# Performance work log

Measured on AMD Instinct MI355X. Metric: run time of the kernel, lower is better.

The kernel has to match this reference:

```python
import jax, jax.numpy as jnp
import numpy as np

D_MODEL = 1024
N_HEADS = 16
NUM_KV_HEADS = 4
D_K = D_MODEL // N_HEADS
ROPE_BASE = 10000.0


def apply_rotary_emb(x, base):
    # x: (B, H, T, d) ; rotate interleaved pairs (x[2i], x[2i+1])
    B, H, T, d = x.shape
    inv_freq = 1.0 / (base ** (jnp.arange(0, d, 2, dtype=jnp.float32) / d))  # (d/2,)
    angles = jnp.arange(T, dtype=jnp.float32)[:, None] * inv_freq[None, :]   # (T, d/2)
    cos = jnp.cos(angles)[None, None]  # (1,1,T,d/2)
    sin = jnp.sin(angles)[None, None]
    x1 = x[..., 0::2]
    x2 = x[..., 1::2]
    out = jnp.stack([x1 * cos - x2 * sin, x1 * sin + x2 * cos], axis=-1)
    return out.reshape(B, H, T, d)


def setup_inputs() -> dict:
    key = jax.random.key(0)
    k1, k2, k3, k4, k5 = jax.random.split(key, 5)
    B, T = 4, 2048
    s = 1.0 / np.sqrt(D_MODEL)
    return {
        "x": jax.random.normal(k1, (B, T, D_MODEL), dtype=jnp.float32),
        "attention_mask": jnp.ones((B, T), dtype=jnp.int32),
        "Wq": jax.random.uniform(k2, (D_MODEL, D_MODEL), jnp.float32, -s, s),
        "Wk": jax.random.uniform(k3, (D_MODEL, NUM_KV_HEADS * D_K), jnp.float32, -s, s),
        "Wv": jax.random.uniform(k4, (D_MODEL, NUM_KV_HEADS * D_K), jnp.float32, -s, s),
        "Wo": jax.random.uniform(k5, (D_MODEL, D_MODEL), jnp.float32, -s, s),
    }


def reference(x, attention_mask, Wq, Wk, Wv, Wo):
    B, T, _ = x.shape
    # QKV projections -> (B, H, T, d_k)
    Q = (x @ Wq).reshape(B, T, N_HEADS, D_K).transpose(0, 2, 1, 3)
    K = (x @ Wk).reshape(B, T, NUM_KV_HEADS, D_K).transpose(0, 2, 1, 3)
    V = (x @ Wv).reshape(B, T, NUM_KV_HEADS, D_K).transpose(0, 2, 1, 3)
    # RoPE on Q and K
    Q = apply_rotary_emb(Q, ROPE_BASE)
    K = apply_rotary_emb(K, ROPE_BASE)
    # GQA expansion: repeat kv heads to match query heads
    rep = N_HEADS // NUM_KV_HEADS
    K = jnp.repeat(K, rep, axis=1)
    V = jnp.repeat(V, rep, axis=1)
    # mask: causal AND query-position padding (faithful to source's pad[:,None,:,None])
    causal = jnp.tril(jnp.ones((T, T), dtype=bool))[None, None]        # (1,1,T,T)
    pad = attention_mask.astype(bool)[:, None, :, None]                 # (B,1,T,1)
    mask = pad & causal                                                 # (B,1,T,T)
    scale = 1.0 / np.sqrt(D_K)
    scores = jnp.einsum("bhqd,bhkd->bhqk", Q, K) * scale
    scores = jnp.where(mask, scores, jnp.finfo(scores.dtype).min)
    attn = jax.nn.softmax(scores, axis=-1)
    out = jnp.einsum("bhqk,bhkd->bhqd", attn, V)                       # (B,H,T,d_k)
    out = out.transpose(0, 2, 1, 3).reshape(B, T, D_MODEL)
    return out @ Wo
```

## Files before the change

### kernel.cpp

```cpp
#include <hip/hip_runtime.h>
#include <hip/hip_bf16.h>


#define B_   4
#define T_   2048
#define DM   1024
#define NH   16
#define NKV  4
#define DK   64
#define BT   (B_ * T_)
#define DKV  (NKV * DK)

typedef __attribute__((ext_vector_type(4))) short s4;
typedef __attribute__((ext_vector_type(8))) short s8;
typedef __attribute__((ext_vector_type(4))) float f4;
typedef __attribute__((ext_vector_type(16))) float f16x;

#define L2E    1.4426950408889634f
#define L2_1E4 0.41524101186092307f

__device__ __forceinline__ unsigned short f2bf(float f) {
    __hip_bfloat16 h = __float2bfloat16(f);
    unsigned short u; __builtin_memcpy(&u, &h, 2); return u;
}
__device__ __forceinline__ float bf2f(unsigned short u) {
    __hip_bfloat16 h; __builtin_memcpy(&h, &u, 2); return __bfloat162float(h);
}

__device__ __forceinline__ float ldf(const void* p, size_t i, bool f32) {
    return f32 ? ((const float*)p)[i]
               : __bfloat162float(((const __hip_bfloat16*)p)[i]);
}
__device__ __forceinline__ bool world_f32(const int* flag) {
    return __builtin_amdgcn_readfirstlane(flag[0]) == 0;
}

__device__ __forceinline__ void async_cp16(const unsigned short* g, unsigned short* l) {
    __builtin_amdgcn_global_load_lds(
        (const __attribute__((address_space(1))) void*)g,
        (__attribute__((address_space(3))) void*)l,
        16, 0, 0);
}

__global__ void probe_fmt(const unsigned int* __restrict__ x, int* __restrict__ flag)
{
    __shared__ int cnt;
    if (threadIdx.x == 0) cnt = 0;
    __syncthreads();
    int local = 0;
    #pragma unroll
    for (int i = 0; i < 16; ++i) {
        unsigned int w  = x[threadIdx.x * 16 + i];
        unsigned int lo = w & 0xFFFFu;
        unsigned int e  = (lo >> 7) & 0xFFu;
        if ((lo & 0x7FFFu) == 0u || (e >= 96u && e <= 144u)) ++local;
    }
    atomicAdd(&cnt, local);
    __syncthreads();
    if (threadIdx.x == 0) flag[0] = (cnt >= 3072) ? 1 : 0;
}

__global__ __launch_bounds__(256) void cvt_x(const float* __restrict__ x,
                                             unsigned short* __restrict__ xb,
                                             const int* __restrict__ flag)
{
    if (!world_f32(flag)) return;
    const size_t i = ((size_t)blockIdx.x * 256 + threadIdx.x) * 8;
    f4 a = *(const f4*)(x + i);
    f4 b = *(const f4*)(x + i + 4);
    unsigned short h[8] = { f2bf(a.x), f2bf(a.y), f2bf(a.z), f2bf(a.w),
                            f2bf(b.x), f2bf(b.y), f2bf(b.z), f2bf(b.w) };
    __builtin_memcpy(xb + i, h, 16);
}

__global__ __launch_bounds__(256) void transp2(const void* __restrict__ W0,
                                               const void* __restrict__ W1,
                                               unsigned short* __restrict__ T0,
                                               unsigned short* __restrict__ T1,
                                               int K, int N,
                                               const int* __restrict__ flag)
{
    const bool f32 = world_f32(flag);
    __shared__ unsigned short Tl[32][33];
    const void* W = blockIdx.z ? W1 : W0;
    unsigned short* T = blockIdx.z ? T1 : T0;
    const int n0 = blockIdx.x * 32, k0 = blockIdx.y * 32;
    const int tx = threadIdx.x & 31, ty = threadIdx.x >> 5;
    #pragma unroll
    for (int i = 0; i < 4; ++i)
        Tl[ty + 8 * i][tx] = f2bf(ldf(W, (size_t)(k0 + ty + 8 * i) * N + n0 + tx, f32));
    __syncthreads();
    #pragma unroll
    for (int i = 0; i < 4; ++i)
        T[(size_t)(n0 + ty + 8 * i) * K + k0 + tx] = Tl[tx][ty + 8 * i];
}

__global__ __launch_bounds__(256) void gemm_bt(const unsigned short* __restrict__ A0,
                                               const unsigned short* __restrict__ A1,
                                               const unsigned short* __restrict__ Bt,
                                               void* __restrict__ C,
                                               void* __restrict__ C2,
                                               int M, int N, int K,
                                               const int* __restrict__ flag,
                                               int mode, float rope_scale)
{
    const unsigned short* Ab = world_f32(flag) ? A1 : A0;

    __shared__ unsigned short Al[3][128 * 32];
    __shared__ unsigned short Bl[3][128 * 32];

    const int tid  = threadIdx.x;
    const int bm   = blockIdx.y * 128;
    const int bn   = blockIdx.x * 128;
    const int w    = tid >> 6;
    const int lane = tid & 63;
    const int qd   = lane >> 4;
    const int ln   = lane & 15;
    const int wm   = (w & 1) * 64;
    const int wn   = (w >> 1) * 64;
    const int sr   = tid >> 2;
    const int sk   = (tid & 3) * 8;

#define STAGE(bb, k0_) {                                                                 \
    async_cp16(Ab + (size_t)(bm + sr) * K + (k0_) + sk,      &Al[bb][tid * 8]);          \
    async_cp16(Ab + (size_t)(bm + 64 + sr) * K + (k0_) + sk, &Al[bb][2048 + tid * 8]);   \
    async_cp16(Bt + (size_t)(bn + sr) * K + (k0_) + sk,      &Bl[bb][tid * 8]);          \
    async_cp16(Bt + (size_t)(bn + 64 + sr) * K + (k0_) + sk, &Bl[bb][2048 + tid * 8]);   \
}

    f4 zero = {0.f, 0.f, 0.f, 0.f};
    f4 acc[4][4];
    #pragma unroll
    for (int i = 0; i < 4; ++i)
        #pragma unroll
        for (int j = 0; j < 4; ++j) acc[i][j] = zero;

    const int NS = K >> 5;
    STAGE(0, 0)
    STAGE(1, 32)
    for (int s = 0; s < NS; ++s) {
        const int cur = s % 3;
        if (s + 1 < NS) asm volatile("s_waitcnt vmcnt(4)" ::: "memory");
        else            asm volatile("s_waitcnt vmcnt(0)" ::: "memory");
        if (s + 2 < NS) { STAGE((s + 2) % 3, (s + 2) << 5) }
        asm volatile("s_barrier" ::: "memory");

        s8 af[4], bfr[4];
        #pragma unroll
        for (int i = 0; i < 4; ++i)
            af[i] = *(const s8*)&Al[cur][(wm + 16 * i + ln) * 32 + qd * 8];
        #pragma unroll
        for (int j = 0; j < 4; ++j)
            bfr[j] = *(const s8*)&Bl[cur][(wn + 16 * j + ln) * 32 + qd * 8];
        #pragma unroll
        for (int i = 0; i < 4; ++i)
            #pragma unroll
            for (int j = 0; j < 4; ++j)
                acc[i][j] = __builtin_amdgcn_mfma_f32_16x16x32_bf16(af[i], bfr[j], acc[i][j], 0, 0, 0);
        asm volatile("s_barrier" ::: "memory");
    }
#undef STAGE

    if (mode == 3) {
        #pragma unroll
        for (int j = 0; j < 4; ++j) {
            const int col = bn + wn + 16 * j + ln;
            if (col < 1280) {
                const float scale = (col < 1024) ? rope_scale : 1.0f;
                const int pr = (col >> 1) & 31;
                const float invf = exp2f(-(float)pr * L2_1E4);
                const bool odd = col & 1;
                #pragma unroll
                for (int i = 0; i < 4; ++i)
                    #pragma unroll
                    for (int r = 0; r < 4; ++r) {
                        const int row = bm + wm + 16 * i + qd * 4 + r;
                        float v = acc[i][j][r];
                        float pv = __shfl_xor(v, 1);
                        float ang = (float)(row & (T_ - 1)) * invf;
                        float sn, cs;
                        __sincosf(ang, &sn, &cs);
                        float out = odd ? (pv * sn + v * cs) : (v * cs - pv * sn);
                        acc[i][j][r] = out * scale;
                    }
            }
        }
    }

    #pragma unroll
    for (int i = 0; i < 4; ++i)
        #pragma unroll
        for (int r = 0; r < 4; ++r) {
            const int row = bm + wm + 16 * i + qd * 4 + r;
            #pragma unroll
            for (int j = 0; j < 4; ++j) {
                const int col = bn + wn + 16 * j + ln;
                const float v = acc[i][j][r];
                if (mode == 0) {
                    ((unsigned short*)C)[(size_t)row * N + col] = f2bf(v);
                } else {
                    if (col < 1024) {
                        ((unsigned short*)C)[(size_t)row * DM + col] = f2bf(v);
                    } else {
                        unsigned short* kv = (unsigned short*)C2 +
                            (col < 1280 ? 0 : (size_t)BT * DKV);
                        kv[(size_t)row * DKV + (col & 255)] = f2bf(v);
                    }
                }
            }
        }
}

__global__ __launch_bounds__(256, 3) void attn_mfma(unsigned short* __restrict__ QO,
                                                    const unsigned short* __restrict__ Kg,
                                                    const unsigned short* __restrict__ Vg)
{
    __shared__ unsigned short Kl[64][72];
    __shared__ unsigned short Vl[64][72];

    const int ip   = blockIdx.x;
    const int bh   = blockIdx.y;
    const int b    = bh >> 4;
    const int h    = bh & 15;
    const int hkv  = h >> 2;
    const int tid  = threadIdx.x;
    const int w    = tid >> 6;
    const int lane = tid & 63;
    const int q    = lane & 31;
    const int hl   = lane >> 5;

    const int rk = tid >> 2, dk = (tid & 3) * 16;
    const int kp = tid & 31, vd0 = (tid >> 5) * 8;
    const unsigned short* kptr = Kg + (size_t)(b * T_ + rk) * DKV + hkv * DK + dk;
    const unsigned short* vptr = Vg + (size_t)(b * T_ + 2 * kp) * DKV + hkv * DK + vd0;

    #pragma unroll 1
    for (int seg = 0; seg < 2; ++seg) {
        const int qt    = seg ? ip : (15 - ip);
        const int qb    = qt * 128;
        const int ktmax = 2 * qt + 1;

        uint4 kra0 = ((const uint4*)kptr)[0];
        uint4 kra1 = ((const uint4*)kptr)[1];
        uint4 vra0 = *(const uint4*)vptr;
        uint4 vra1 = *(const uint4*)(vptr + DKV);

        s8 qf[4];
        {
            const unsigned short* Qp =
                QO + (size_t)(b * T_ + qb + 32 * w + q) * DM + h * DK + 8 * hl;
            #pragma unroll
            for (int s = 0; s < 4; ++s)
                qf[s] = *(const s8*)(Qp + 16 * s);
        }

        const int qmaxw = qb + 32 * w + 31;
        const int qglob = qb + 32 * w + q;

        f16x O0, O1;
        #pragma unroll
        for (int r = 0; r < 16; ++r) { O0[r] = 0.f; O1[r] = 0.f; }
        float lsumA = 0.f, lsumB = 0.f;

        for (int kt = 0; kt <= ktmax; ++kt) {
            *(uint4*)&Kl[rk][dk]     = kra0;
            *(uint4*)&Kl[rk][dk + 8] = kra1;
            {
                const unsigned short* lo = (const unsigned short*)&vra0;
                const unsigned short* hi = (const unsigned short*)&vra1;
                #pragma unroll
                for (int i = 0; i < 8; ++i)
                    *(unsigned int*)&Vl[vd0 + i][2 * kp] =
                        (unsigned int)lo[i] | ((unsigned int)hi[i] << 16);
            }
            if (kt < ktmax) {
                const size_t o = (size_t)(kt + 1) * 64 * DKV;
                kra0 = ((const uint4*)(kptr + o))[0];
                kra1 = ((const uint4*)(kptr + o))[1];
                vra0 = *(const uint4*)(vptr + o);
                vra1 = *(const uint4*)(vptr + o + DKV);
            }
            asm volatile("s_waitcnt lgkmcnt(0)\n\ts_barrier" ::: "memory");

            const int kb = kt * 64;
            if (kb <= qmaxw) {
                f16x S0, S1;
                #pragma unroll
                for (int r = 0; r < 16; ++r) { S0[r] = 0.f; S1[r] = 0.f; }
                #pragma unroll
                for (int s = 0; s < 4; ++s) {
                    s8 k0 = *(const s8*)&Kl[q][16 * s + 8 * hl];
                    s8 k1 = *(const s8*)&Kl[32 + q][16 * s + 8 * hl];
                    S0 = __builtin_amdgcn_mfma_f32_32x32x16_bf16(k0, qf[s], S0, 0, 0, 0);
                    S1 = __builtin_amdgcn_mfma_f32_32x32x16_bf16(k1, qf[s], S1, 0, 0, 0);
                }

                unsigned pk0[8], pk1[8];
                const bool full = (kb + 63 <= qb + 32 * w);
                if (full) {
                    #pragma unroll
                    for (int j = 0; j < 8; ++j) {
                        float a0 = exp2f(S0[2 * j]), a1 = exp2f(S0[2 * j + 1]);
                        float c0 = exp2f(S1[2 * j]), c1 = exp2f(S1[2 * j + 1]);
                        lsumA += a0 + a1;
                        lsumB += c0 + c1;
                        pk0[j] = (unsigned)f2bf(a0) | ((unsigned)f2bf(a1) << 16);
                        pk1[j] = (unsigned)f2bf(c0) | ((unsigned)f2bf(c1) << 16);
                    }
                } else {
                    #pragma unroll
                    for (int j = 0; j < 8; ++j) {
                        const int r0 = 2 * j;
                        const int key0 = kb + (r0 & 3) + 8 * (r0 >> 2) + 4 * hl;
                        float a0 = (key0      <= qglob) ? exp2f(S0[r0])     : 0.f;
                        float a1 = (key0 + 1  <= qglob) ? exp2f(S0[r0 + 1]) : 0.f;
                        float c0 = (key0 + 32 <= qglob) ? exp2f(S1[r0])     : 0.f;
                        float c1 = (key0 + 33 <= qglob) ? exp2f(S1[r0 + 1]) : 0.f;
                        lsumA += a0 + a1;
                        lsumB += c0 + c1;
                        pk0[j] = (unsigned)f2bf(a0) | ((unsigned)f2bf(a1) << 16);
                        pk1[j] = (unsigned)f2bf(c0) | ((unsigned)f2bf(c1) << 16);
                    }
                }

                #define PV_STEP(PG, KS) {                                          \
                    const unsigned a0 = PG[4 * ((KS) & 1) + 0];                    \
                    const unsigned a1 = PG[4 * ((KS) & 1) + 1];                    \
                    const unsigned a2 = PG[4 * ((KS) & 1) + 2];                    \
                    const unsigned a3 = PG[4 * ((KS) & 1) + 3];                    \
                    const unsigned own0 = hl ? a2 : a0;                            \
                    const unsigned own1 = hl ? a3 : a1;                            \
                    const unsigned xs0  = hl ? a0 : a2;                            \
                    const unsigned xs1  = hl ? a1 : a3;                            \
                    const unsigned xa = (unsigned)__shfl_xor((int)xs0, 32);        \
                    const unsigned xb = (unsigned)__shfl_xor((int)xs1, 32);        \
                    unsigned dw[4];                                                \
                    dw[0] = hl ? xa : own0;                                        \
                    dw[1] = hl ? xb : own1;                                        \
                    dw[2] = hl ? own0 : xa;                                        \
                    dw[3] = hl ? own1 : xb;                                        \
                    s8 pf; __builtin_memcpy(&pf, dw, 16);                          \
                    s8 v0 = *(const s8*)&Vl[q][16 * (KS) + 8 * hl];                \
                    s8 v1 = *(const s8*)&Vl[32 + q][16 * (KS) + 8 * hl];           \
                    O0 = __builtin_amdgcn_mfma_f32_32x32x16_bf16(v0, pf, O0, 0, 0, 0); \
                    O1 = __builtin_amdgcn_mfma_f32_32x32x16_bf16(v1, pf, O1, 0, 0, 0); \
                }
                PV_STEP(pk0, 0)
                PV_STEP(pk0, 1)
                PV_STEP(pk1, 2)
                PV_STEP(pk1, 3)
                #undef PV_STEP
            }
            asm volatile("s_barrier" ::: "memory");
        }

        const float lsum = lsumA + lsumB;
        const float lf = lsum + __shfl_xor(lsum, 32);
        const float inv = 1.0f / lf;
        unsigned short* Op = QO + (size_t)(b * T_ + qb + 32 * w + q) * DM + h * DK;
        #pragma unroll
        for (int g2 = 0; g2 < 2; ++g2) {
            #pragma unroll
            for (int rq = 0; rq < 4; ++rq) {
                const int d0 = 32 * g2 + 8 * rq + 4 * hl;
                const float o0 = (g2 ? O1[4 * rq + 0] : O0[4 * rq + 0]) * inv;
                const float o1 = (g2 ? O1[4 * rq + 1] : O0[4 * rq + 1]) * inv;
                const float o2 = (g2 ? O1[4 * rq + 2] : O0[4 * rq + 2]) * inv;
                const float o3 = (g2 ? O1[4 * rq + 3] : O0[4 * rq + 3]) * inv;
                unsigned out2[2] = {
                    (unsigned)f2bf(o0) | ((unsigned)f2bf(o1) << 16),
                    (unsigned)f2bf(o2) | ((unsigned)f2bf(o3) << 16) };
                __builtin_memcpy(Op + d0, out2, 8);
            }
        }
    }
}

__global__ __launch_bounds__(256) void copy_out(const unsigned short* __restrict__ Cb,
                                                void* __restrict__ out,
                                                const int* __restrict__ flag)
{
    const bool f32 = world_f32(flag);
    size_t i = ((size_t)blockIdx.x * 256 + threadIdx.x) * 8;
    uint4 v = *(const uint4*)(Cb + i);
    if (!f32) {
        *(uint4*)((unsigned short*)out + i) = v;
    } else {
        const unsigned short* u = (const unsigned short*)&v;
        float* o = (float*)out + i;
        #pragma unroll
        for (int k = 0; k < 8; ++k) o[k] = bf2f(u[k]);
    }
}

extern "C" void kernel_launch(void* const* d_in, const int* in_sizes, int n_in,
                              void* d_out, int out_size, void* d_ws, size_t ws_size,
                              hipStream_t stream)
{
    const void* x  = d_in[0];
    const void* Wq = d_in[2];
    const void* Wk = d_in[3];
    const void* Wv = d_in[4];
    const void* Wo = d_in[5];

    int* flag = (int*)d_ws;
    unsigned short* WqkvT = (unsigned short*)((char*)d_ws + 4096);
    unsigned short* WoT   = WqkvT + (size_t)1536 * DM;
    unsigned short* Kb    = WoT + (size_t)DM * DM;
    unsigned short* Vb    = Kb + (size_t)BT * DKV;
    unsigned short* Cb    = Kb;

    unsigned short* Qb = (unsigned short*)d_out;
    unsigned short* xb = (unsigned short*)d_out + (size_t)BT * DM;

    dim3 blk(256);

    probe_fmt<<<1, blk, 0, stream>>>((const unsigned int*)x, flag);

    cvt_x<<<dim3(BT * DM / 2048), blk, 0, stream>>>((const float*)x, xb, flag);

    transp2<<<dim3(32, 32, 2), blk, 0, stream>>>(Wq, Wo, WqkvT, WoT, DM, DM, flag);
    transp2<<<dim3(8, 32, 2), blk, 0, stream>>>(
        Wk, Wv, WqkvT + (size_t)1024 * DM, WqkvT + (size_t)1280 * DM, DM, DKV, flag);

    gemm_bt<<<dim3(1536 / 128, BT / 128), blk, 0, stream>>>(
        (const unsigned short*)x, xb, WqkvT, Qb, Kb, BT, 1536, DM, flag, 3, 0.125f * L2E);

    attn_mfma<<<dim3(T_ / 256, B_ * NH), blk, 0, stream>>>(Qb, Kb, Vb);

    gemm_bt<<<dim3(DM / 128, BT / 128), blk, 0, stream>>>(
        Qb, Qb, WoT, Cb, nullptr, BT, DM, DM, flag, 0, 1.0f);
    copy_out<<<dim3(BT * DM / 2048), blk, 0, stream>>>(Cb, d_out, flag);
}
```

Measured before the change: 264.9 us.

## Retile projection GEMMs to 256x256 blocks with 512 threads and k64 double buffering

Replaces the 128x128, 256-thread GEMM (three-stage pipeline over k=32 steps) with a 256x256, 512-thread kernel. Each wave now computes a 128x64 sub-tile, and the kernel double-buffers k=64 slabs in LDS. The aim is more data reuse per LDS load and fewer barrier and pipeline steps per unit of MFMA work. The cost is about 128KB of LDS per block and far fewer blocks: 192 for the QKV GEMM and 128 for the output GEMM. That likely leaves many CUs idle and limits latency hiding to one block per CU.

```diff
diff --git a/kernel.cpp b/kernel.cpp
--- a/kernel.cpp
+++ b/kernel.cpp
@@ -95,86 +95,91 @@
         T[(size_t)(n0 + ty + 8 * i) * K + k0 + tx] = Tl[tx][ty + 8 * i];
 }
 
-__global__ __launch_bounds__(256) void gemm_bt(const unsigned short* __restrict__ A0,
-                                               const unsigned short* __restrict__ A1,
-                                               const unsigned short* __restrict__ Bt,
-                                               void* __restrict__ C,
-                                               void* __restrict__ C2,
-                                               int M, int N, int K,
-                                               const int* __restrict__ flag,
-                                               int mode, float rope_scale)
+__global__ __launch_bounds__(512, 2) void gemm256(const unsigned short* __restrict__ A0,
+                                                  const unsigned short* __restrict__ A1,
+                                                  const unsigned short* __restrict__ Bt,
+                                                  void* __restrict__ C,
+                                                  void* __restrict__ C2,
+                                                  int M, int N, int K,
+                                                  const int* __restrict__ flag,
+                                                  int mode, float rope_scale)
 {
     const unsigned short* Ab = world_f32(flag) ? A1 : A0;
 
-    __shared__ unsigned short Al[3][128 * 32];
-    __shared__ unsigned short Bl[3][128 * 32];
+    __shared__ unsigned short Al[2][256 * 64];
+    __shared__ unsigned short Bl[2][256 * 64];
 
     const int tid  = threadIdx.x;
-    const int bm   = blockIdx.y * 128;
-    const int bn   = blockIdx.x * 128;
+    const int bm   = blockIdx.y * 256;
+    const int bn   = blockIdx.x * 256;
     const int w    = tid >> 6;
+    const int wm   = w >> 2;
+    const int wn   = w & 3;
     const int lane = tid & 63;
     const int qd   = lane >> 4;
     const int ln   = lane & 15;
-    const int wm   = (w & 1) * 64;
-    const int wn   = (w >> 1) * 64;
     const int sr   = tid >> 2;
     const int sk   = (tid & 3) * 8;
 
-#define STAGE(bb, k0_) {                                                                 \
-    async_cp16(Ab + (size_t)(bm + sr) * K + (k0_) + sk,      &Al[bb][tid * 8]);          \
-    async_cp16(Ab + (size_t)(bm + 64 + sr) * K + (k0_) + sk, &Al[bb][2048 + tid * 8]);   \
-    async_cp16(Bt + (size_t)(bn + sr) * K + (k0_) + sk,      &Bl[bb][tid * 8]);          \
-    async_cp16(Bt + (size_t)(bn + 64 + sr) * K + (k0_) + sk, &Bl[bb][2048 + tid * 8]);   \
+#define STAGE(bb, k0_) {                                                                        \
+    async_cp16(Ab + (size_t)(bm + sr) * K + (k0_) + sk,            &Al[bb][sr * 32 + sk]);              \
+    async_cp16(Ab + (size_t)(bm + 128 + sr) * K + (k0_) + sk,      &Al[bb][4096 + sr * 32 + sk]);       \
+    async_cp16(Ab + (size_t)(bm + sr) * K + (k0_) + 32 + sk,       &Al[bb][8192 + sr * 32 + sk]);       \
+    async_cp16(Ab + (size_t)(bm + 128 + sr) * K + (k0_) + 32 + sk, &Al[bb][12288 + sr * 32 + sk]);      \
+    async_cp16(Bt + (size_t)(bn + sr) * K + (k0_) + sk,            &Bl[bb][sr * 32 + sk]);              \
+    async_cp16(Bt + (size_t)(bn + 128 + sr) * K + (k0_) + sk,      &Bl[bb][4096 + sr * 32 + sk]);       \
+    async_cp16(Bt + (size_t)(bn + sr) * K + (k0_) + 32 + sk,       &Bl[bb][8192 + sr * 32 + sk]);       \
+    async_cp16(Bt + (size_t)(bn + 128 + sr) * K + (k0_) + 32 + sk, &Bl[bb][12288 + sr * 32 + sk]);      \
 }
 
     f4 zero = {0.f, 0.f, 0.f, 0.f};
-    f4 acc[4][4];
+    f4 acc[8][4];
     #pragma unroll
-    for (int i = 0; i < 4; ++i)
+    for (int i = 0; i < 8; ++i)
         #pragma unroll
         for (int j = 0; j < 4; ++j) acc[i][j] = zero;
 
-    const int NS = K >> 5;
+    const int NT = K >> 6;
     STAGE(0, 0)
-    STAGE(1, 32)
-    for (int s = 0; s < NS; ++s) {
-        const int cur = s % 3;
-        if (s + 1 < NS) asm volatile("s_waitcnt vmcnt(4)" ::: "memory");
-        else            asm volatile("s_waitcnt vmcnt(0)" ::: "memory");
-        if (s + 2 < NS) { STAGE((s + 2) % 3, (s + 2) << 5) }
+    for (int t = 0; t < NT; ++t) {
+        const int cur = t & 1;
+        asm volatile("s_waitcnt vmcnt(0)" ::: "memory");
         asm volatile("s_barrier" ::: "memory");
-
-        s8 af[4], bfr[4];
-        #pragma unroll
-        for (int i = 0; i < 4; ++i)
-            af[i] = *(const s8*)&Al[cur][(wm + 16 * i + ln) * 32 + qd * 8];
-        #pragma unroll
-        for (int j = 0; j < 4; ++j)
-            bfr[j] = *(const s8*)&Bl[cur][(wn + 16 * j + ln) * 32 + qd * 8];
-        #pragma unroll
-        for (int i = 0; i < 4; ++i)
+        if (t + 1 < NT) { STAGE(cur ^ 1, (t + 1) << 6) }
+
+        s8 bfr[2][4];
+        #pragma unroll
+        for (int ksub = 0; ksub < 2; ++ksub)
             #pragma unroll
             for (int j = 0; j < 4; ++j)
-                acc[i][j] = __builtin_amdgcn_mfma_f32_16x16x32_bf16(af[i], bfr[j], acc[i][j], 0, 0, 0);
-        asm volatile("s_barrier" ::: "memory");
+                bfr[ksub][j] = *(const s8*)&Bl[cur][ksub * 8192 + (wn * 64 + 16 * j + ln) * 32 + qd * 8];
+        #pragma unroll
+        for (int i = 0; i < 8; ++i) {
+            s8 a0 = *(const s8*)&Al[cur][          (wm * 128 + 16 * i + ln) * 32 + qd * 8];
+            s8 a1 = *(const s8*)&Al[cur][8192 + (wm * 128 + 16 * i + ln) * 32 + qd * 8];
+            #pragma unroll
+            for (int j = 0; j < 4; ++j) {
+                acc[i][j] = __builtin_amdgcn_mfma_f32_16x16x32_bf16(a0, bfr[0][j], acc[i][j], 0, 0, 0);
+                acc[i][j] = __builtin_amdgcn_mfma_f32_16x16x32_bf16(a1, bfr[1][j], acc[i][j], 0, 0, 0);
+            }
+        }
     }
 #undef STAGE
 
     if (mode == 3) {
         #pragma unroll
         for (int j = 0; j < 4; ++j) {
-            const int col = bn + wn + 16 * j + ln;
+            const int col = bn + wn * 64 + 16 * j + ln;
             if (col < 1280) {
                 const float scale = (col < 1024) ? rope_scale : 1.0f;
                 const int pr = (col >> 1) & 31;
                 const float invf = exp2f(-(float)pr * L2_1E4);
                 const bool odd = col & 1;
                 #pragma unroll
-                for (int i = 0; i < 4; ++i)
+                for (int i = 0; i < 8; ++i)
                     #pragma unroll
                     for (int r = 0; r < 4; ++r) {
-                        const int row = bm + wm + 16 * i + qd * 4 + r;
+                        const int row = bm + wm * 128 + 16 * i + qd * 4 + r;
                         float v = acc[i][j][r];
                         float pv = __shfl_xor(v, 1);
                         float ang = (float)(row & (T_ - 1)) * invf;
@@ -188,13 +193,13 @@
     }
 
     #pragma unroll
-    for (int i = 0; i < 4; ++i)
+    for (int i = 0; i < 8; ++i)
         #pragma unroll
         for (int r = 0; r < 4; ++r) {
-            const int row = bm + wm + 16 * i + qd * 4 + r;
+            const int row = bm + wm * 128 + 16 * i + qd * 4 + r;
             #pragma unroll
             for (int j = 0; j < 4; ++j) {
-                const int col = bn + wn + 16 * j + ln;
+                const int col = bn + wn * 64 + 16 * j + ln;
                 const float v = acc[i][j][r];
                 if (mode == 0) {
                     ((unsigned short*)C)[(size_t)row * N + col] = f2bf(v);
@@ -423,12 +428,12 @@
     transp2<<<dim3(8, 32, 2), blk, 0, stream>>>(
         Wk, Wv, WqkvT + (size_t)1024 * DM, WqkvT + (size_t)1280 * DM, DM, DKV, flag);
 
-    gemm_bt<<<dim3(1536 / 128, BT / 128), blk, 0, stream>>>(
+    gemm256<<<dim3(1536 / 256, BT / 256), dim3(512), 0, stream>>>(
         (const unsigned short*)x, xb, WqkvT, Qb, Kb, BT, 1536, DM, flag, 3, 0.125f * L2E);
 
     attn_mfma<<<dim3(T_ / 256, B_ * NH), blk, 0, stream>>>(Qb, Kb, Vb);
 
-    gemm_bt<<<dim3(DM / 128, BT / 128), blk, 0, stream>>>(
+    gemm256<<<dim3(DM / 256, BT / 256), dim3(512), 0, stream>>>(
         Qb, Qb, WoT, Cb, nullptr, BT, DM, DM, flag, 0, 1.0f);
     copy_out<<<dim3(BT * DM / 2048), blk, 0, stream>>>(Cb, d_out, flag);
 }
```

Result: slower. 292.5 us (+10.4%).

## Split long causal query tiles across blocks with partial-sum combine kernel

Applied to the files above, without the earlier changes.

Replaces the paired-segment attention schedule with a 22-slot work table per (batch, head). The largest query tiles (10-15) are split over two blocks that each process half the key range and write unnormalized fp32 partial outputs and row sums, which a new combine kernel adds and normalizes. The occupancy hint rises from 3 to 5 blocks per CU. The aim is better load balance and more parallelism across CUs, at the cost of extra fp32 scratch traffic, an extra launch, and workspace reuse of the weight and x buffers. Splitting only happens on the fp32 input path; otherwise the split slots exit early.

```diff
diff --git a/kernel.cpp b/kernel.cpp
--- a/kernel.cpp
+++ b/kernel.cpp
@@ -211,18 +211,39 @@
         }
 }
 
-__global__ __launch_bounds__(256, 3) void attn_mfma(unsigned short* __restrict__ QO,
+__global__ __launch_bounds__(256, 5) void attn_mfma(unsigned short* __restrict__ QO,
                                                     const unsigned short* __restrict__ Kg,
-                                                    const unsigned short* __restrict__ Vg)
+                                                    const unsigned short* __restrict__ Vg,
+                                                    const int* __restrict__ flag,
+                                                    float* __restrict__ pA,
+                                                    float* __restrict__ pB,
+                                                    float* __restrict__ lA,
+                                                    float* __restrict__ lB)
 {
     __shared__ unsigned short Kl[64][72];
     __shared__ unsigned short Vl[64][72];
 
-    const int ip   = blockIdx.x;
-    const int bh   = blockIdx.y;
+    const int TQT[22]  = {9,8,15,15,7,14,14,13,13,6,12,12,11,11,5,10,10,4,3,2,1,0};
+    const int TLO[22]  = {0,0,0,16,0,0,15,0,14,0,0,13,0,12,0,0,11,0,0,0,0,0};
+    const int THI[22]  = {19,17,15,31,15,14,29,13,27,13,12,25,11,23,11,10,21,9,7,5,3,1};
+    const int TMODE[22]= {0,0,1,2,0,1,2,1,2,0,1,2,1,2,0,1,2,0,0,0,0,0};
+
+    const bool wf32 = world_f32(flag);
+    const int bh   = blockIdx.x;
+    const int slot = blockIdx.y;
+    const int qt   = TQT[slot];
+    const int lo   = TLO[slot];
+    int hi   = THI[slot];
+    int mode = TMODE[slot];
+    if (!wf32) {
+        if (mode == 2) return;
+        if (mode == 1) { hi = 2 * qt + 1; mode = 0; }
+    }
+
     const int b    = bh >> 4;
     const int h    = bh & 15;
     const int hkv  = h >> 2;
+    const int qb   = qt * 128;
     const int tid  = threadIdx.x;
     const int w    = tid >> 6;
     const int lane = tid & 63;
@@ -231,131 +252,126 @@
 
     const int rk = tid >> 2, dk = (tid & 3) * 16;
     const int kp = tid & 31, vd0 = (tid >> 5) * 8;
-    const unsigned short* kptr = Kg + (size_t)(b * T_ + rk) * DKV + hkv * DK + dk;
-    const unsigned short* vptr = Vg + (size_t)(b * T_ + 2 * kp) * DKV + hkv * DK + vd0;
-
-    #pragma unroll 1
-    for (int seg = 0; seg < 2; ++seg) {
-        const int qt    = seg ? ip : (15 - ip);
-        const int qb    = qt * 128;
-        const int ktmax = 2 * qt + 1;
-
-        uint4 kra0 = ((const uint4*)kptr)[0];
-        uint4 kra1 = ((const uint4*)kptr)[1];
-        uint4 vra0 = *(const uint4*)vptr;
-        uint4 vra1 = *(const uint4*)(vptr + DKV);
-
-        s8 qf[4];
+    const unsigned short* kptr = Kg + (size_t)(b * T_ + lo * 64 + rk) * DKV + hkv * DK + dk;
+    const unsigned short* vptr = Vg + (size_t)(b * T_ + lo * 64 + 2 * kp) * DKV + hkv * DK + vd0;
+
+    uint4 kra0 = ((const uint4*)kptr)[0];
+    uint4 kra1 = ((const uint4*)kptr)[1];
+    uint4 vra0 = *(const uint4*)vptr;
+    uint4 vra1 = *(const uint4*)(vptr + DKV);
+
+    s8 qf[4];
+    {
+        const unsigned short* Qp =
+            QO + (size_t)(b * T_ + qb + 32 * w + q) * DM + h * DK + 8 * hl;
+        #pragma unroll
+        for (int s = 0; s < 4; ++s)
+            qf[s] = *(const s8*)(Qp + 16 * s);
+    }
+
+    const int qmaxw = qb + 32 * w + 31;
+    const int qglob = qb + 32 * w + q;
+
+    f16x O0, O1;
+    #pragma unroll
+    for (int r = 0; r < 16; ++r) { O0[r] = 0.f; O1[r] = 0.f; }
+    float lsumA = 0.f, lsumB = 0.f;
+
+    for (int kt = lo; kt <= hi; ++kt) {
+        *(uint4*)&Kl[rk][dk]     = kra0;
+        *(uint4*)&Kl[rk][dk + 8] = kra1;
         {
-            const unsigned short* Qp =
-                QO + (size_t)(b * T_ + qb + 32 * w + q) * DM + h * DK + 8 * hl;
-            #pragma unroll
-            for (int s = 0; s < 4; ++s)
-                qf[s] = *(const s8*)(Qp + 16 * s);
-        }
-
-        const int qmaxw = qb + 32 * w + 31;
-        const int qglob = qb + 32 * w + q;
-
-        f16x O0, O1;
-        #pragma unroll
-        for (int r = 0; r < 16; ++r) { O0[r] = 0.f; O1[r] = 0.f; }
-        float lsumA = 0.f, lsumB = 0.f;
-
-        for (int kt = 0; kt <= ktmax; ++kt) {
-            *(uint4*)&Kl[rk][dk]     = kra0;
-            *(uint4*)&Kl[rk][dk + 8] = kra1;
-            {
-                const unsigned short* lo = (const unsigned short*)&vra0;
-                const unsigned short* hi = (const unsigned short*)&vra1;
+            const unsigned short* lov = (const unsigned short*)&vra0;
+            const unsigned short* hiv = (const unsigned short*)&vra1;
+            #pragma unroll
+            for (int i = 0; i < 8; ++i)
+                *(unsigned int*)&Vl[vd0 + i][2 * kp] =
+                    (unsigned int)lov[i] | ((unsigned int)hiv[i] << 16);
+        }
+        if (kt < hi) {
+            const size_t o = (size_t)(kt + 1 - lo) * 64 * DKV;
+            kra0 = ((const uint4*)(kptr + o))[0];
+            kra1 = ((const uint4*)(kptr + o))[1];
+            vra0 = *(const uint4*)(vptr + o);
+            vra1 = *(const uint4*)(vptr + o + DKV);
+        }
+        asm volatile("s_waitcnt lgkmcnt(0)\n\ts_barrier" ::: "memory");
+
+        const int kb = kt * 64;
+        if (kb <= qmaxw) {
+            f16x S0, S1;
+            #pragma unroll
+            for (int r = 0; r < 16; ++r) { S0[r] = 0.f; S1[r] = 0.f; }
+            #pragma unroll
+            for (int s = 0; s < 4; ++s) {
+                s8 k0 = *(const s8*)&Kl[q][16 * s + 8 * hl];
+                s8 k1 = *(const s8*)&Kl[32 + q][16 * s + 8 * hl];
+                S0 = __builtin_amdgcn_mfma_f32_32x32x16_bf16(k0, qf[s], S0, 0, 0, 0);
+                S1 = __builtin_amdgcn_mfma_f32_32x32x16_bf16(k1, qf[s], S1, 0, 0, 0);
+            }
+
+            unsigned pk0[8], pk1[8];
+            const bool full = (kb + 63 <= qb + 32 * w);
+            if (full) {
                 #pragma unroll
-                for (int i = 0; i < 8; ++i)
-                    *(unsigned int*)&Vl[vd0 + i][2 * kp] =
-                        (unsigned int)lo[i] | ((unsigned int)hi[i] << 16);
-            }
-            if (kt < ktmax) {
-                const size_t o = (size_t)(kt + 1) * 64 * DKV;
-                kra0 = ((const uint4*)(kptr + o))[0];
-                kra1 = ((const uint4*)(kptr + o))[1];
-                vra0 = *(const uint4*)(vptr + o);
-                vra1 = *(const uint4*)(vptr + o + DKV);
-            }
-            asm volatile("s_waitcnt lgkmcnt(0)\n\ts_barrier" ::: "memory");
-
-            const int kb = kt * 64;
-            if (kb <= qmaxw) {
-                f16x S0, S1;
+                for (int j = 0; j < 8; ++j) {
+                    float a0 = exp2f(S0[2 * j]), a1 = exp2f(S0[2 * j + 1]);
+                    float c0 = exp2f(S1[2 * j]), c1 = exp2f(S1[2 * j + 1]);
+                    lsumA += a0 + a1;
+                    lsumB += c0 + c1;
+                    pk0[j] = (unsigned)f2bf(a0) | ((unsigned)f2bf(a1) << 16);
+                    pk1[j] = (unsigned)f2bf(c0) | ((unsigned)f2bf(c1) << 16);
+                }
+            } else {
                 #pragma unroll
-                for (int r = 0; r < 16; ++r) { S0[r] = 0.f; S1[r] = 0.f; }
-                #pragma unroll
-                for (int s = 0; s < 4; ++s) {
-                    s8 k0 = *(const s8*)&Kl[q][16 * s + 8 * hl];
-                    s8 k1 = *(const s8*)&Kl[32 + q][16 * s + 8 * hl];
-                    S0 = __builtin_amdgcn_mfma_f32_32x32x16_bf16(k0, qf[s], S0, 0, 0, 0);
-                    S1 = __builtin_amdgcn_mfma_f32_32x32x16_bf16(k1, qf[s], S1, 0, 0, 0);
+                for (int j = 0; j < 8; ++j) {
+                    const int r0 = 2 * j;
+                    const int key0 = kb + (r0 & 3) + 8 * (r0 >> 2) + 4 * hl;
+                    float a0 = (key0      <= qglob) ? exp2f(S0[r0])     : 0.f;
+                    float a1 = (key0 + 1  <= qglob) ? exp2f(S0[r0 + 1]) : 0.f;
+                    float c0 = (key0 + 32 <= qglob) ? exp2f(S1[r0])     : 0.f;
+                    float c1 = (key0 + 33 <= qglob) ? exp2f(S1[r0 + 1]) : 0.f;
+                    lsumA += a0 + a1;
+                    lsumB += c0 + c1;
+                    pk0[j] = (unsigned)f2bf(a0) | ((unsigned)f2bf(a1) << 16);
+                    pk1[j] = (unsigned)f2bf(c0) | ((unsigned)f2bf(c1) << 16);
                 }
-
-                unsigned pk0[8], pk1[8];
-                const bool full = (kb + 63 <= qb + 32 * w);
-                if (full) {
-                    #pragma unroll
-                    for (int j = 0; j < 8; ++j) {
-                        float a0 = exp2f(S0[2 * j]), a1 = exp2f(S0[2 * j + 1]);
-                        float c0 = exp2f(S1[2 * j]), c1 = exp2f(S1[2 * j + 1]);
-                        lsumA += a0 + a1;
-                        lsumB += c0 + c1;
-                        pk0[j] = (unsigned)f2bf(a0) | ((unsigned)f2bf(a1) << 16);
-                        pk1[j] = (unsigned)f2bf(c0) | ((unsigned)f2bf(c1) << 16);
-                    }
-                } else {
-                    #pragma unroll
-                    for (int j = 0; j < 8; ++j) {
-                        const int r0 = 2 * j;
-                        const int key0 = kb + (r0 & 3) + 8 * (r0 >> 2) + 4 * hl;
-                        float a0 = (key0      <= qglob) ? exp2f(S0[r0])     : 0.f;
-                        float a1 = (key0 + 1  <= qglob) ? exp2f(S0[r0 + 1]) : 0.f;
-                        float c0 = (key0 + 32 <= qglob) ? exp2f(S1[r0])     : 0.f;
-                        float c1 = (key0 + 33 <= qglob) ? exp2f(S1[r0 + 1]) : 0.f;
-                        lsumA += a0 + a1;
-                        lsumB += c0 + c1;
-                        pk0[j] = (unsigned)f2bf(a0) | ((unsigned)f2bf(a1) << 16);
-                        pk1[j] = (unsigned)f2bf(c0) | ((unsigned)f2bf(c1) << 16);
-                    }
-                }
-
-                #define PV_STEP(PG, KS) {                                          \
-                    const unsigned a0 = PG[4 * ((KS) & 1) + 0];                    \
-                    const unsigned a1 = PG[4 * ((KS) & 1) + 1];                    \
-                    const unsigned a2 = PG[4 * ((KS) & 1) + 2];                    \
-                    const unsigned a3 = PG[4 * ((KS) & 1) + 3];                    \
-                    const unsigned own0 = hl ? a2 : a0;                            \
-                    const unsigned own1 = hl ? a3 : a1;                            \
-                    const unsigned xs0  = hl ? a0 : a2;                            \
-                    const unsigned xs1  = hl ? a1 : a3;                            \
-                    const unsigned xa = (unsigned)__shfl_xor((int)xs0, 32);        \
-                    const unsigned xb = (unsigned)__shfl_xor((int)xs1, 32);        \
-                    unsigned dw[4];                                                \
-                    dw[0] = hl ? xa : own0;                                        \
-                    dw[1] = hl ? xb : own1;                                        \
-                    dw[2] = hl ? own0 : xa;                                        \
-                    dw[3] = hl ? own1 : xb;                                        \
-                    s8 pf; __builtin_memcpy(&pf, dw, 16);                          \
-                    s8 v0 = *(const s8*)&Vl[q][16 * (KS) + 8 * hl];                \
-                    s8 v1 = *(const s8*)&Vl[32 + q][16 * (KS) + 8 * hl];           \
-                    O0 = __builtin_amdgcn_mfma_f32_32x32x16_bf16(v0, pf, O0, 0, 0, 0); \
-                    O1 = __builtin_amdgcn_mfma_f32_32x32x16_bf16(v1, pf, O1, 0, 0, 0); \
-                }
-                PV_STEP(pk0, 0)
-                PV_STEP(pk0, 1)
-                PV_STEP(pk1, 2)
-                PV_STEP(pk1, 3)
-                #undef PV_STEP
-            }
-            asm volatile("s_barrier" ::: "memory");
-        }
-
-        const float lsum = lsumA + lsumB;
-        const float lf = lsum + __shfl_xor(lsum, 32);
+            }
+
+            #define PV_STEP(PG, KS) {                                          \
+                const unsigned a0 = PG[4 * ((KS) & 1) + 0];                    \
+                const unsigned a1 = PG[4 * ((KS) & 1) + 1];                    \
+                const unsigned a2 = PG[4 * ((KS) & 1) + 2];                    \
+                const unsigned a3 = PG[4 * ((KS) & 1) + 3];                    \
+                const unsigned own0 = hl ? a2 : a0;                            \
+                const unsigned own1 = hl ? a3 : a1;                            \
+                const unsigned xs0  = hl ? a0 : a2;                            \
+                const unsigned xs1  = hl ? a1 : a3;                            \
+                const unsigned xa = (unsigned)__shfl_xor((int)xs0, 32);        \
+                const unsigned xb2 = (unsigned)__shfl_xor((int)xs1, 32);       \
+                unsigned dw[4];                                                \
+                dw[0] = hl ? xa : own0;                                        \
+                dw[1] = hl ? xb2 : own1;                                       \
+                dw[2] = hl ? own0 : xa;                                        \
+                dw[3] = hl ? own1 : xb2;                                       \
+                s8 pf; __builtin_memcpy(&pf, dw, 16);                          \
+                s8 v0 = *(const s8*)&Vl[q][16 * (KS) + 8 * hl];                \
+                s8 v1 = *(const s8*)&Vl[32 + q][16 * (KS) + 8 * hl];           \
+                O0 = __builtin_amdgcn_mfma_f32_32x32x16_bf16(v0, pf, O0, 0, 0, 0); \
+                O1 = __builtin_amdgcn_mfma_f32_32x32x16_bf16(v1, pf, O1, 0, 0, 0); \
+            }
+            PV_STEP(pk0, 0)
+            PV_STEP(pk0, 1)
+            PV_STEP(pk1, 2)
+            PV_STEP(pk1, 3)
+            #undef PV_STEP
+        }
+        asm volatile("s_barrier" ::: "memory");
+    }
+
+    const float lsum = lsumA + lsumB;
+    const float lf = lsum + __shfl_xor(lsum, 32);
+    if (mode == 0) {
         const float inv = 1.0f / lf;
         unsigned short* Op = QO + (size_t)(b * T_ + qb + 32 * w + q) * DM + h * DK;
         #pragma unroll
@@ -373,7 +389,51 @@
                 __builtin_memcpy(Op + d0, out2, 8);
             }
         }
-    }
+    } else {
+        const int sidx = qt - 10;
+        const int rg = bh * 768 + sidx * 128 + (32 * w + q);
+        float* P = (mode == 1 ? pA : pB) + ((size_t)rg << 6);
+        #pragma unroll
+        for (int g2 = 0; g2 < 2; ++g2) {
+            #pragma unroll
+            for (int rq = 0; rq < 4; ++rq) {
+                const int d0 = 32 * g2 + 8 * rq + 4 * hl;
+                f4 vv = { (g2 ? O1[4 * rq + 0] : O0[4 * rq + 0]),
+                          (g2 ? O1[4 * rq + 1] : O0[4 * rq + 1]),
+                          (g2 ? O1[4 * rq + 2] : O0[4 * rq + 2]),
+                          (g2 ? O1[4 * rq + 3] : O0[4 * rq + 3]) };
+                *(f4*)(P + d0) = vv;
+            }
+        }
+        if (hl == 0) (mode == 1 ? lA : lB)[rg] = lf;
+    }
+}
+
+__global__ __launch_bounds__(256) void combine(const float* __restrict__ pA,
+                                               const float* __restrict__ pB,
+                                               const float* __restrict__ lA,
+                                               const float* __restrict__ lB,
+                                               unsigned short* __restrict__ Qb,
+                                               const int* __restrict__ flag)
+{
+    if (!world_f32(flag)) return;
+    const int idx = blockIdx.x * 256 + threadIdx.x;
+    const int rg = idx >> 3, ch = idx & 7;
+    const float inv = 1.0f / (lA[rg] + lB[rg]);
+    const float* a = pA + ((size_t)rg << 6) + ch * 8;
+    const float* c = pB + ((size_t)rg << 6) + ch * 8;
+    f4 u0 = *(const f4*)a, u1 = *(const f4*)(a + 4);
+    f4 v0 = *(const f4*)c, v1 = *(const f4*)(c + 4);
+    unsigned out2[4] = {
+        (unsigned)f2bf((u0.x + v0.x) * inv) | ((unsigned)f2bf((u0.y + v0.y) * inv) << 16),
+        (unsigned)f2bf((u0.z + v0.z) * inv) | ((unsigned)f2bf((u0.w + v0.w) * inv) << 16),
+        (unsigned)f2bf((u1.x + v1.x) * inv) | ((unsigned)f2bf((u1.y + v1.y) * inv) << 16),
+        (unsigned)f2bf((u1.z + v1.z) * inv) | ((unsigned)f2bf((u1.w + v1.w) * inv) << 16) };
+    const int bh = rg / 768, rem = rg % 768;
+    const int s = rem >> 7, r = rem & 127;
+    const int b = bh >> 4, h = bh & 15;
+    const size_t off = (size_t)(b * T_ + (s + 10) * 128 + r) * DM + h * DK + ch * 8;
+    __builtin_memcpy(Qb + off, out2, 16);
 }
 
 __global__ __launch_bounds__(256) void copy_out(const unsigned short* __restrict__ Cb,
@@ -404,14 +464,18 @@
     const void* Wo = d_in[5];
 
     int* flag = (int*)d_ws;
-    unsigned short* WqkvT = (unsigned short*)((char*)d_ws + 4096);
-    unsigned short* WoT   = WqkvT + (size_t)1536 * DM;
+    unsigned short* WoT   = (unsigned short*)((char*)d_ws + 4096);
     unsigned short* Kb    = WoT + (size_t)DM * DM;
     unsigned short* Vb    = Kb + (size_t)BT * DKV;
-    unsigned short* Cb    = Kb;
+    unsigned short* WqkvT = Vb + (size_t)BT * DKV;
+    float* pB = (float*)WqkvT;
+    float* lA = (float*)((char*)WqkvT + 12582912);
+    float* lB = lA + 49152;
+    unsigned short* Cb = Kb;
 
     unsigned short* Qb = (unsigned short*)d_out;
     unsigned short* xb = (unsigned short*)d_out + (size_t)BT * DM;
+    float* pA = (float*)xb;
 
     dim3 blk(256);
 
@@ -426,7 +490,8 @@
     gemm_bt<<<dim3(1536 / 128, BT / 128), blk, 0, stream>>>(
         (const unsigned short*)x, xb, WqkvT, Qb, Kb, BT, 1536, DM, flag, 3, 0.125f * L2E);
 
-    attn_mfma<<<dim3(T_ / 256, B_ * NH), blk, 0, stream>>>(Qb, Kb, Vb);
+    attn_mfma<<<dim3(B_ * NH, 22), blk, 0, stream>>>(Qb, Kb, Vb, flag, pA, pB, lA, lB);
+    combine<<<dim3(1536), blk, 0, stream>>>(pA, pB, lA, lB, Qb, flag);
 
     gemm_bt<<<dim3(DM / 128, BT / 128), blk, 0, stream>>>(
         Qb, Qb, WoT, Cb, nullptr, BT, DM, DM, flag, 0, 1.0f);
```

After: 355.3 us. 34.1% more time.
